# Kernel optimization log

Hardware: AMD Instinct MI355X
Metric: run time of the kernel (lower is better)

## Reference

```python
import jax, jax.numpy as jnp
import numpy as np
import math

B, S, D, H, DK = 4, 2048, 512, 8, 64

def _xavier(key, shape):
    fan_in, fan_out = shape[-2], shape[-1]
    std = math.sqrt(2.0 / (fan_in + fan_out))
    return jax.random.normal(key, shape, dtype=jnp.float32) * std

def setup_inputs() -> dict:
    key = jax.random.key(0)
    ks = jax.random.split(key, 5)
    X = jax.random.normal(ks[0], (B, S, D), dtype=jnp.float32)
    W_q = _xavier(ks[1], (H, D, DK))
    W_k = _xavier(ks[2], (H, D, DK))
    W_v = _xavier(ks[3], (H, D, DK))
    W_o = _xavier(ks[4], (H * DK, D))
    return {"X": X, "W_q": W_q, "W_k": W_k, "W_v": W_v, "W_o": W_o}

def reference(X, W_q, W_k, W_v, W_o):
    d_k = W_q.shape[-1]
    # project all heads at once: [B,H,S,dk]
    Q = jnp.einsum('bsd,hdk->bhsk', X, W_q)
    K = jnp.einsum('bsd,hdk->bhsk', X, W_k)
    V = jnp.einsum('bsd,hdk->bhsk', X, W_v)
    scores = jnp.einsum('bhsk,bhtk->bhst', Q, K) / jnp.sqrt(jnp.asarray(d_k, X.dtype))
    seq_len = X.shape[1]
    causal = jnp.tril(jnp.ones((seq_len, seq_len), dtype=bool))  # strict upper -> -inf
    scores = jnp.where(causal[None, None, :, :], scores, -jnp.inf)
    attn = jax.nn.softmax(scores, axis=-1)
    out = jnp.einsum('bhst,bhtk->bhsk', attn, V)  # [B,H,S,dv]
    # original concat order: permute to (B,S,dv,H) then flatten -> head axis fastest
    Bx, Hx, Sx, DV = out.shape
    concat = jnp.transpose(out, (0, 2, 3, 1)).reshape(Bx, Sx, DV * Hx)
    return jnp.matmul(concat, W_o)
```

## Files before the change

### kernel.cpp

```cpp
#include <hip/hip_runtime.h>
#include <hip/hip_bf16.h>


typedef __bf16 bf16;
typedef __bf16 bf16x8 __attribute__((ext_vector_type(8)));
typedef __bf16 bf16x4 __attribute__((ext_vector_type(4)));
typedef __bf16 bf16x2 __attribute__((ext_vector_type(2)));
typedef float  f32x4  __attribute__((ext_vector_type(4)));
typedef float  f32x16 __attribute__((ext_vector_type(16)));
typedef unsigned int u32;
typedef u32 u32x4 __attribute__((ext_vector_type(4)));

#define AS1 __attribute__((address_space(1)))
#define AS3 __attribute__((address_space(3)))

__device__ __forceinline__ void async_lds16(const void* gsrc, void* ldst) {
  __builtin_amdgcn_global_load_lds((AS1 const void*)gsrc, (AS3 void*)ldst, 16, 0, 0);
}

__device__ __forceinline__ float fexp2(float x) {
  float r;
  asm("v_exp_f32 %0, %1" : "=v"(r) : "v"(x));
  return r;
}


__global__ __launch_bounds__(256) void k_cvt_x(const float4* __restrict__ X,
                                               bf16x4* __restrict__ Xb) {
  int i = blockIdx.x * 256 + threadIdx.x;
  float4 v = X[i];
  bf16x4 o = { (bf16)v.x, (bf16)v.y, (bf16)v.z, (bf16)v.w };
  Xb[i] = o;
}

__global__ __launch_bounds__(256) void k_build_w(const float* __restrict__ Wq,
                                                 const float* __restrict__ Wk,
                                                 const float* __restrict__ Wv,
                                                 const float* __restrict__ Wo,
                                                 bf16* __restrict__ BT,
                                                 bf16* __restrict__ WoT) {
  int idx = blockIdx.x * 256 + threadIdx.x;
  if (idx < 786432) {
    int n = idx >> 9, d = idx & 511;
    int which = n >> 9, h = (n >> 6) & 7, dk = n & 63;
    const float* W = (which == 0) ? Wq : ((which == 1) ? Wk : Wv);
    BT[idx] = (bf16)W[((h << 9) + d) * 64 + dk];
  } else {
    int i2 = idx - 786432;
    int d = i2 >> 9, c = i2 & 511;
    int h = c >> 6, dk = c & 63;
    WoT[i2] = (bf16)Wo[(((dk << 3) + h) << 9) + d];
  }
}


__device__ __forceinline__ void gemm_tile(const bf16* __restrict__ A,
                                          const bf16* __restrict__ BT,
                                          int K, int m0, int n0,
                                          char* sm, f32x4 acc[4][4]) {
  const int tid = threadIdx.x;
  const int lane = tid & 63, w = tid >> 6;
  const int wm = w >> 1, wn = w & 1;
  const int lr = lane & 15, lg = lane >> 4;
#define GSTAGE(bi, k0) do {                                                        \
    char* base_ = sm + ((bi) << 14);                                               \
    _Pragma("unroll")                                                              \
    for (int i_ = 0; i_ < 2; ++i_) {                                               \
      int off_ = i_ * 256 + tid;                                                   \
      int row_ = off_ >> 2, cb_ = (off_ & 3) << 4;                                 \
      async_lds16((const char*)(A  + (m0 + row_) * K + (k0)) + cb_,                \
                  base_ + off_ * 16);                                              \
      async_lds16((const char*)(BT + (n0 + row_) * K + (k0)) + cb_,                \
                  base_ + 8192 + off_ * 16);                                       \
    }                                                                              \
  } while (0)
  const int NT = K >> 5;
  GSTAGE(0, 0);
  asm volatile("s_waitcnt vmcnt(0)" ::: "memory");
  __builtin_amdgcn_s_barrier();
  __builtin_amdgcn_sched_barrier(0);
  for (int t = 0; t < NT; ++t) {
    char* cb = sm + ((t & 1) << 14);
    if (t + 1 < NT) GSTAGE((t + 1) & 1, (t + 1) << 5);
    bf16x8 af[4], bfr[4];
    #pragma unroll
    for (int u = 0; u < 4; ++u) {
      af[u]  = *(const bf16x8*)(cb +        ((wm * 64 + u * 16 + lr) * 32 + 8 * lg) * 2);
      bfr[u] = *(const bf16x8*)(cb + 8192 + ((wn * 64 + u * 16 + lr) * 32 + 8 * lg) * 2);
    }
    __builtin_amdgcn_s_setprio(1);
    #pragma unroll
    for (int am = 0; am < 4; ++am)
      #pragma unroll
      for (int bn = 0; bn < 4; ++bn)
        acc[am][bn] = __builtin_amdgcn_mfma_f32_16x16x32_bf16(af[am], bfr[bn], acc[am][bn], 0, 0, 0);
    __builtin_amdgcn_s_setprio(0);
    if (t + 1 < NT) {
      asm volatile("s_waitcnt vmcnt(0)" ::: "memory");
      __builtin_amdgcn_s_barrier();
      __builtin_amdgcn_sched_barrier(0);
    }
  }
#undef GSTAGE
}

__global__ __launch_bounds__(256) void k_gemm_qkv(const bf16* __restrict__ A,
                                                  const bf16* __restrict__ BT,
                                                  bf16* __restrict__ Qb,
                                                  bf16* __restrict__ Kb,
                                                  bf16* __restrict__ VTb) {
  __shared__ char sm[32768];
  const int m0 = blockIdx.y * 128, n0 = blockIdx.x * 128;
  f32x4 acc[4][4];
  #pragma unroll
  for (int a = 0; a < 4; ++a)
    #pragma unroll
    for (int b = 0; b < 4; ++b) { f32x4 z = {0.f,0.f,0.f,0.f}; acc[a][b] = z; }
  gemm_tile(A, BT, 512, m0, n0, sm, acc);
  const int lane = threadIdx.x & 63, w = threadIdx.x >> 6;
  const int wm = w >> 1, wn = w & 1, lr = lane & 15, lg = lane >> 4;
  const float qsc = 0.1803368801f;
  #pragma unroll
  for (int am = 0; am < 4; ++am)
    #pragma unroll
    for (int bn = 0; bn < 4; ++bn)
      #pragma unroll
      for (int r = 0; r < 4; ++r) {
        int m = m0 + wm * 64 + am * 16 + 4 * lg + r;
        int n = n0 + wn * 64 + bn * 16 + lr;
        int b = m >> 11, s = m & 2047;
        int which = n >> 9, h = (n >> 6) & 7, dk = n & 63;
        int bh = (b << 3) + h;
        float x = acc[am][bn][r];
        if (which == 0)      Qb[((bh << 11) + s) * 64 + dk] = (bf16)(x * qsc);
        else if (which == 1) Kb[((bh << 11) + s) * 64 + dk] = (bf16)x;
        else                 VTb[((bh << 6) + dk) * 2048 + s] = (bf16)x;
      }
}

__global__ __launch_bounds__(256) void k_gemm_out(const bf16* __restrict__ A,
                                                  const bf16* __restrict__ BT,
                                                  float* __restrict__ C) {
  __shared__ char sm[32768];
  const int m0 = blockIdx.y * 128, n0 = blockIdx.x * 128;
  f32x4 acc[4][4];
  #pragma unroll
  for (int a = 0; a < 4; ++a)
    #pragma unroll
    for (int b = 0; b < 4; ++b) { f32x4 z = {0.f,0.f,0.f,0.f}; acc[a][b] = z; }
  gemm_tile(A, BT, 512, m0, n0, sm, acc);
  const int lane = threadIdx.x & 63, w = threadIdx.x >> 6;
  const int wm = w >> 1, wn = w & 1, lr = lane & 15, lg = lane >> 4;
  #pragma unroll
  for (int am = 0; am < 4; ++am)
    #pragma unroll
    for (int bn = 0; bn < 4; ++bn)
      #pragma unroll
      for (int r = 0; r < 4; ++r) {
        int m = m0 + wm * 64 + am * 16 + 4 * lg + r;
        int n = n0 + wn * 64 + bn * 16 + lr;
        C[(m << 9) + n] = acc[am][bn][r];
      }
}


__device__ __forceinline__ void attn_stage(char* base, const bf16* Kh, const bf16* Vh,
                                           int tb, int tid) {
  #pragma unroll
  for (int k = 0; k < 2; ++k) {
    int s = tid + (k << 8);
    int row = s >> 3, g = s & 7;
    async_lds16((const void*)(Kh + ((tb + row) << 6) + ((g ^ (row & 7)) << 3)),
                base + s * 16);
  }
  #pragma unroll
  for (int k = 0; k < 2; ++k) {
    int s = tid + (k << 8);
    int row = s >> 3, g = s & 7;
    async_lds16((const void*)(Vh + (row << 11) + tb + ((g ^ (row & 7)) << 3)),
                base + 8192 + s * 16);
  }
}

__global__ __launch_bounds__(256, 2) void k_attn6(const bf16* __restrict__ Qb,
                                                  const bf16* __restrict__ Kb,
                                                  const bf16* __restrict__ VTb,
                                                  bf16* __restrict__ Oc) {
  __shared__ char sm[32768];
  const int tid = threadIdx.x, lane = tid & 63, wv = tid >> 6;
  const int l31 = lane & 31, hi = lane >> 5;
  const int bid = blockIdx.x;
  const int bh = bid & 31;
  const int qb = (bid < 256) ? (15 - (bid >> 5)) : ((bid - 256) >> 5);
  const int b = bh >> 3, h = bh & 7;
  const int q0 = qb << 7;
  const int wq0 = q0 + (wv << 5);
  const bf16* Qh = Qb  + ((size_t)bh << 17);
  const bf16* Kh = Kb  + ((size_t)bh << 17);
  const bf16* Vh = VTb + ((size_t)bh << 17);

  bf16x8 qf[4];
  #pragma unroll
  for (int kd = 0; kd < 4; ++kd)
    qf[kd] = *(const bf16x8*)(Qh + ((wq0 + l31) << 6) + kd * 16 + 8 * hi);

  f32x16 o0, o1;
  #pragma unroll
  for (int r = 0; r < 16; ++r) { o0[r] = 0.f; o1[r] = 0.f; }
  float m_run = -3e38f, lsum = 0.f;

  const int NT = (qb << 1) + 2;
  const int swz = l31 & 7;

  attn_stage(sm, Kh, Vh, 0, tid);

  for (int t = 0; t < NT; ++t) {
    const int tb = t << 6;
    char* cb = sm + ((t & 1) << 14);
    __syncthreads();
    if (t + 1 < NT)
      attn_stage(sm + (((t + 1) & 1) << 14), Kh, Vh, (t + 1) << 6, tid);
    if (tb > wq0 + 31) continue;

    f32x16 sA, sB;
    #pragma unroll
    for (int r = 0; r < 16; ++r) { sA[r] = 0.f; sB[r] = 0.f; }
    {
      bf16x8 kf[4];
      #pragma unroll
      for (int kd = 0; kd < 4; ++kd)
        kf[kd] = *(const bf16x8*)(cb + l31 * 128 + ((((kd << 1) + hi) ^ swz) << 4));
      __builtin_amdgcn_s_setprio(1);
      #pragma unroll
      for (int kd = 0; kd < 4; ++kd)
        sA = __builtin_amdgcn_mfma_f32_32x32x16_bf16(kf[kd], qf[kd], sA, 0, 0, 0);
      __builtin_amdgcn_s_setprio(0);
      #pragma unroll
      for (int kd = 0; kd < 4; ++kd)
        kf[kd] = *(const bf16x8*)(cb + (32 + l31) * 128 + ((((kd << 1) + hi) ^ swz) << 4));
      __builtin_amdgcn_s_setprio(1);
      #pragma unroll
      for (int kd = 0; kd < 4; ++kd)
        sB = __builtin_amdgcn_mfma_f32_32x32x16_bf16(kf[kd], qf[kd], sB, 0, 0, 0);
      __builtin_amdgcn_s_setprio(0);
    }

    const int sg = wq0 + l31;
    if (tb + 63 > wq0) {
      #pragma unroll
      for (int r = 0; r < 16; ++r) {
        int rk = tb + (r & 3) + 8 * (r >> 2) + 4 * hi;
        sA[r] = (rk > sg)      ? -1e30f : sA[r];
        sB[r] = (rk + 32 > sg) ? -1e30f : sB[r];
      }
    }
    float tv[16];
    #pragma unroll
    for (int r = 0; r < 16; ++r) tv[r] = fmaxf(sA[r], sB[r]);
    float m0_ = fmaxf(tv[0], tv[1]),  m1_ = fmaxf(tv[2], tv[3]);
    float m2_ = fmaxf(tv[4], tv[5]),  m3_ = fmaxf(tv[6], tv[7]);
    float m4_ = fmaxf(tv[8], tv[9]),  m5_ = fmaxf(tv[10], tv[11]);
    float m6_ = fmaxf(tv[12], tv[13]), m7_ = fmaxf(tv[14], tv[15]);
    float tmax = fmaxf(fmaxf(fmaxf(m0_, m1_), fmaxf(m2_, m3_)),
                       fmaxf(fmaxf(m4_, m5_), fmaxf(m6_, m7_)));
    float tms = fmaxf(tmax, __shfl_xor(tmax, 32));
    if (!__all(tms <= m_run + 8.f)) {
      float mn = fmaxf(m_run, tms);
      float fac = fexp2(m_run - mn);
      #pragma unroll
      for (int r = 0; r < 16; ++r) { o0[r] *= fac; o1[r] *= fac; }
      lsum *= fac;
      m_run = mn;
    }
    #pragma unroll
    for (int r = 0; r < 16; ++r) sA[r] = fexp2(sA[r] - m_run);
    #pragma unroll
    for (int r = 0; r < 16; ++r) sB[r] = fexp2(sB[r] - m_run);
    float a0 = (sA[0]+sB[0]) + (sA[1]+sB[1]),   a1 = (sA[2]+sB[2]) + (sA[3]+sB[3]);
    float a2 = (sA[4]+sB[4]) + (sA[5]+sB[5]),   a3 = (sA[6]+sB[6]) + (sA[7]+sB[7]);
    float a4 = (sA[8]+sB[8]) + (sA[9]+sB[9]),   a5 = (sA[10]+sB[10]) + (sA[11]+sB[11]);
    float a6 = (sA[12]+sB[12]) + (sA[13]+sB[13]), a7 = (sA[14]+sB[14]) + (sA[15]+sB[15]);
    float rs = ((a0 + a1) + (a2 + a3)) + ((a4 + a5) + (a6 + a7));
    lsum += rs + __shfl_xor(rs, 32);

    #pragma unroll
    for (int j = 0; j < 2; ++j) {
      u32 pk_[8];
      #pragma unroll
      for (int i = 0; i < 8; ++i) {
        float plo = j ? sB[2 * i] : sA[2 * i];
        float phi = j ? sB[2 * i + 1] : sA[2 * i + 1];
        bf16x2 pr = { (bf16)plo, (bf16)phi };
        pk_[i] = __builtin_bit_cast(u32, pr);
      }
      asm volatile("v_permlane32_swap_b32 %0, %1" : "+v"(pk_[0]), "+v"(pk_[2]));
      asm volatile("v_permlane32_swap_b32 %0, %1" : "+v"(pk_[1]), "+v"(pk_[3]));
      asm volatile("v_permlane32_swap_b32 %0, %1" : "+v"(pk_[4]), "+v"(pk_[6]));
      asm volatile("v_permlane32_swap_b32 %0, %1" : "+v"(pk_[5]), "+v"(pk_[7]));
      u32x4 w0 = { pk_[0], pk_[1], pk_[2], pk_[3] };
      u32x4 w1 = { pk_[4], pk_[5], pk_[6], pk_[7] };
      bf16x8 pb0 = __builtin_bit_cast(bf16x8, w0);
      bf16x8 pb1 = __builtin_bit_cast(bf16x8, w1);
      const char* vb = cb + 8192;
      bf16x8 v00 = *(const bf16x8*)(vb + l31 * 128        + ((((j << 2) + hi) ^ swz) << 4));
      bf16x8 v01 = *(const bf16x8*)(vb + l31 * 128        + ((((j << 2) + 2 + hi) ^ swz) << 4));
      bf16x8 v10 = *(const bf16x8*)(vb + (32 + l31) * 128 + ((((j << 2) + hi) ^ swz) << 4));
      bf16x8 v11 = *(const bf16x8*)(vb + (32 + l31) * 128 + ((((j << 2) + 2 + hi) ^ swz) << 4));
      __builtin_amdgcn_s_setprio(1);
      o0 = __builtin_amdgcn_mfma_f32_32x32x16_bf16(v00, pb0, o0, 0, 0, 0);
      o0 = __builtin_amdgcn_mfma_f32_32x32x16_bf16(v01, pb1, o0, 0, 0, 0);
      o1 = __builtin_amdgcn_mfma_f32_32x32x16_bf16(v10, pb0, o1, 0, 0, 0);
      o1 = __builtin_amdgcn_mfma_f32_32x32x16_bf16(v11, pb1, o1, 0, 0, 0);
      __builtin_amdgcn_s_setprio(0);
    }
  }

  float rn = 1.f / lsum;
  const int sg = wq0 + l31;
  bf16* Orow = Oc + (((size_t)((b << 11) + sg)) << 9) + (h << 6);
  #pragma unroll
  for (int g = 0; g < 4; ++g) {
    bf16x4 v0, v1;
    #pragma unroll
    for (int i = 0; i < 4; ++i) {
      v0[i] = (bf16)(o0[4 * g + i] * rn);
      v1[i] = (bf16)(o1[4 * g + i] * rn);
    }
    *(bf16x4*)(Orow + 4 * hi + 8 * g)      = v0;
    *(bf16x4*)(Orow + 32 + 4 * hi + 8 * g) = v1;
  }
}


extern "C" void kernel_launch(void* const* d_in, const int* in_sizes, int n_in,
                              void* d_out, int out_size, void* d_ws, size_t ws_size,
                              hipStream_t stream) {
  (void)in_sizes; (void)n_in; (void)out_size; (void)ws_size;
  const float* X  = (const float*)d_in[0];
  const float* Wq = (const float*)d_in[1];
  const float* Wk = (const float*)d_in[2];
  const float* Wv = (const float*)d_in[3];
  const float* Wo = (const float*)d_in[4];
  float* out = (float*)d_out;
  char* ws = (char*)d_ws;
  bf16* Xb   = (bf16*)(ws);
  bf16* Wqkv = (bf16*)(ws + 8388608);
  bf16* WoT  = (bf16*)(ws + 9961472);
  bf16* Qb   = (bf16*)(ws + 10485760);
  bf16* Kb   = (bf16*)(ws + 18874368);
  bf16* VTb  = (bf16*)(ws + 27262976);
  bf16* Oc   = (bf16*)(ws + 35651584);

  k_cvt_x<<<4096, 256, 0, stream>>>((const float4*)X, (bf16x4*)Xb);
  k_build_w<<<4096, 256, 0, stream>>>(Wq, Wk, Wv, Wo, Wqkv, WoT);
  k_gemm_qkv<<<dim3(12, 64), 256, 0, stream>>>(Xb, Wqkv, Qb, Kb, VTb);
  k_attn6<<<512, 256, 0, stream>>>(Qb, Kb, VTb, Oc);
  k_gemm_out<<<dim3(4, 64), 256, 0, stream>>>(Oc, WoT, out);
}
```

Baseline: 92.47 us.

## Split causal attention KV range in halves with separate combine kernel

Each query block's key range is split into two equal halves processed by separate workgroups (1024 blocks instead of 512), writing unnormalized fp32 partial outputs plus running max and sum. A new combine kernel merges the two partials with log-sum-exp rescaling and writes the bf16 concatenated output. Launch bounds raise the occupancy target to 4 blocks per CU. This balances work across blocks for the causal mask and adds parallelism, at the cost of an extra kernel launch and roughly 33 MB of fp32 partial-result traffic through global memory.

```diff
diff --git a/kernel.cpp b/kernel.cpp
--- a/kernel.cpp
+++ b/kernel.cpp
@@ -182,19 +182,23 @@
   }
 }
 
-__global__ __launch_bounds__(256, 2) void k_attn6(const bf16* __restrict__ Qb,
+__global__ __launch_bounds__(256, 4) void k_attn8(const bf16* __restrict__ Qb,
                                                   const bf16* __restrict__ Kb,
                                                   const bf16* __restrict__ VTb,
-                                                  bf16* __restrict__ Oc) {
+                                                  float* __restrict__ Opart,
+                                                  float* __restrict__ Mpart,
+                                                  float* __restrict__ Lpart) {
   __shared__ char sm[32768];
   const int tid = threadIdx.x, lane = tid & 63, wv = tid >> 6;
   const int l31 = lane & 31, hi = lane >> 5;
   const int bid = blockIdx.x;
   const int bh = bid & 31;
-  const int qb = (bid < 256) ? (15 - (bid >> 5)) : ((bid - 256) >> 5);
-  const int b = bh >> 3, h = bh & 7;
-  const int q0 = qb << 7;
-  const int wq0 = q0 + (wv << 5);
+  const int u = bid >> 5;
+  const int s = 15 - (u >> 1);
+  const int hf = u & 1;
+  const int HL = s + 1;
+  const int t0 = hf * HL;
+  const int wq0 = (s << 7) + (wv << 5);
   const bf16* Qh = Qb  + ((size_t)bh << 17);
   const bf16* Kh = Kb  + ((size_t)bh << 17);
   const bf16* Vh = VTb + ((size_t)bh << 17);
@@ -209,17 +213,16 @@
   for (int r = 0; r < 16; ++r) { o0[r] = 0.f; o1[r] = 0.f; }
   float m_run = -3e38f, lsum = 0.f;
 
-  const int NT = (qb << 1) + 2;
   const int swz = l31 & 7;
 
-  attn_stage(sm, Kh, Vh, 0, tid);
-
-  for (int t = 0; t < NT; ++t) {
-    const int tb = t << 6;
-    char* cb = sm + ((t & 1) << 14);
+  attn_stage(sm, Kh, Vh, t0 << 6, tid);
+
+  for (int tt = 0; tt < HL; ++tt) {
+    const int tb = (t0 + tt) << 6;
+    char* cb = sm + ((tt & 1) << 14);
     __syncthreads();
-    if (t + 1 < NT)
-      attn_stage(sm + (((t + 1) & 1) << 14), Kh, Vh, (t + 1) << 6, tid);
+    if (tt + 1 < HL)
+      attn_stage(sm + (((tt + 1) & 1) << 14), Kh, Vh, (t0 + tt + 1) << 6, tid);
     if (tb > wq0 + 31) continue;
 
     f32x16 sA, sB;
@@ -315,19 +318,51 @@
     }
   }
 
-  float rn = 1.f / lsum;
-  const int sg = wq0 + l31;
-  bf16* Orow = Oc + (((size_t)((b << 11) + sg)) << 9) + (h << 6);
+  const int prow = (wv << 5) + l31;
+  float* Po = Opart + (((size_t)bid) << 13) + (prow << 6);
   #pragma unroll
   for (int g = 0; g < 4; ++g) {
-    bf16x4 v0, v1;
-    #pragma unroll
-    for (int i = 0; i < 4; ++i) {
-      v0[i] = (bf16)(o0[4 * g + i] * rn);
-      v1[i] = (bf16)(o1[4 * g + i] * rn);
-    }
-    *(bf16x4*)(Orow + 4 * hi + 8 * g)      = v0;
-    *(bf16x4*)(Orow + 32 + 4 * hi + 8 * g) = v1;
+    f32x4 w0 = { o0[4*g], o0[4*g+1], o0[4*g+2], o0[4*g+3] };
+    f32x4 w1 = { o1[4*g], o1[4*g+1], o1[4*g+2], o1[4*g+3] };
+    *(f32x4*)(Po + (g << 3) + (hi << 2))      = w0;
+    *(f32x4*)(Po + 32 + (g << 3) + (hi << 2)) = w1;
+  }
+  if (!hi) {
+    Mpart[(bid << 7) + prow] = m_run;
+    Lpart[(bid << 7) + prow] = lsum;
+  }
+}
+
+__global__ __launch_bounds__(256) void k_comb(const float* __restrict__ Opart,
+                                              const float* __restrict__ Mpart,
+                                              const float* __restrict__ Lpart,
+                                              bf16* __restrict__ Oc) {
+  const int bid = blockIdx.x;
+  const int bh = bid & 31, cs = bid >> 5;
+  const int s = 15 - cs;
+  const int pu1 = ((cs << 1) | 0) * 32 + bh;
+  const int pu2 = ((cs << 1) | 1) * 32 + bh;
+  const int b = bh >> 3, h = bh & 7;
+  const int t = threadIdx.x;
+  const int row = t >> 1;
+  const int dh = (t & 1) << 5;
+  float m1 = Mpart[(pu1 << 7) + row], m2 = Mpart[(pu2 << 7) + row];
+  float l1 = Lpart[(pu1 << 7) + row], l2 = Lpart[(pu2 << 7) + row];
+  float mm = fmaxf(m1, m2);
+  float f1 = fexp2(m1 - mm), f2 = fexp2(m2 - mm);
+  float rn = 1.f / (l1 * f1 + l2 * f2);
+  const float* P1 = Opart + (((size_t)pu1) << 13) + (row << 6) + dh;
+  const float* P2 = Opart + (((size_t)pu2) << 13) + (row << 6) + dh;
+  const int sg = (s << 7) + row;
+  bf16* Od = Oc + (((size_t)((b << 11) + sg)) << 9) + (h << 6) + dh;
+  #pragma unroll
+  for (int g = 0; g < 8; ++g) {
+    f32x4 a = *(const f32x4*)(P1 + 4 * g);
+    f32x4 c = *(const f32x4*)(P2 + 4 * g);
+    bf16x4 o;
+    #pragma unroll
+    for (int i = 0; i < 4; ++i) o[i] = (bf16)((a[i] * f1 + c[i] * f2) * rn);
+    *(bf16x4*)(Od + 4 * g) = o;
   }
 }
 
@@ -343,17 +378,21 @@
   const float* Wo = (const float*)d_in[4];
   float* out = (float*)d_out;
   char* ws = (char*)d_ws;
-  bf16* Xb   = (bf16*)(ws);
-  bf16* Wqkv = (bf16*)(ws + 8388608);
-  bf16* WoT  = (bf16*)(ws + 9961472);
-  bf16* Qb   = (bf16*)(ws + 10485760);
-  bf16* Kb   = (bf16*)(ws + 18874368);
-  bf16* VTb  = (bf16*)(ws + 27262976);
-  bf16* Oc   = (bf16*)(ws + 35651584);
+  bf16*  Xb    = (bf16*)(ws);
+  bf16*  Wqkv  = (bf16*)(ws + 8388608);
+  bf16*  WoT   = (bf16*)(ws + 9961472);
+  bf16*  Qb    = (bf16*)(ws + 10485760);
+  bf16*  Kb    = (bf16*)(ws + 18874368);
+  bf16*  VTb   = (bf16*)(ws + 27262976);
+  bf16*  Oc    = (bf16*)(ws + 35651584);
+  float* Opart = (float*)(ws + 44040192);
+  float* Mpart = (float*)(ws + 77594624);
+  float* Lpart = (float*)(ws + 78118912);
 
   k_cvt_x<<<4096, 256, 0, stream>>>((const float4*)X, (bf16x4*)Xb);
   k_build_w<<<4096, 256, 0, stream>>>(Wq, Wk, Wv, Wo, Wqkv, WoT);
   k_gemm_qkv<<<dim3(12, 64), 256, 0, stream>>>(Xb, Wqkv, Qb, Kb, VTb);
-  k_attn6<<<512, 256, 0, stream>>>(Qb, Kb, VTb, Oc);
+  k_attn8<<<1024, 256, 0, stream>>>(Qb, Kb, VTb, Opart, Mpart, Lpart);
+  k_comb<<<512, 256, 0, stream>>>(Opart, Mpart, Lpart, Oc);
   k_gemm_out<<<dim3(4, 64), 256, 0, stream>>>(Oc, WoT, out);
 }
```

Measured after the change: 97.52 us. +5.5%, slower.
